# Kernel tuning notes

Measured on AMD Instinct MI355X. Metric: run time of the kernel, lower is better.

The kernel has to match this reference:

```python
import jax, jax.numpy as jnp
import numpy as np

N_NODES = 50000
N_EDGES = 800000
N_GRAPHS = 512
IN_CH, HID_CH, OUT_CH, N_CLASSES = 128, 64, 64, 10


def gcn_conv(x, src, dst, ew, W, b, n_nodes):
    """PyG GCNConv: add self-loops (weight 1), symmetric normalization, x @ W, scatter-add at dst, + bias."""
    xw = x @ W  # [N, out]
    loop = jnp.arange(n_nodes, dtype=src.dtype)
    src_f = jnp.concatenate([src, loop])
    dst_f = jnp.concatenate([dst, loop])
    ew_f = jnp.concatenate([ew, jnp.ones((n_nodes,), dtype=ew.dtype)])
    deg = jax.ops.segment_sum(ew_f, dst_f, num_segments=n_nodes)  # [N]
    dinv = jnp.where(deg > 0, jax.lax.rsqrt(deg), 0.0)
    norm = dinv[src_f] * ew_f * dinv[dst_f]  # [E+N]
    msg = norm[:, None] * xw[src_f]  # gather + scale
    out = jax.ops.segment_sum(msg, dst_f, num_segments=n_nodes)  # scatter-add
    return out + b


def setup_inputs() -> dict:
    key = jax.random.key(0)
    ks = jax.random.split(key, 12)
    x = jax.random.normal(ks[0], (N_NODES, IN_CH), dtype=jnp.float32)
    edge_index = jax.random.randint(ks[1], (2, N_EDGES), 0, N_NODES, dtype=jnp.int64)
    edge_attr = jax.random.uniform(ks[2], (N_EDGES,), dtype=jnp.float32)
    batch = jnp.sort(jax.random.randint(ks[3], (N_NODES,), 0, N_GRAPHS, dtype=jnp.int64))
    def glorot(k, shape):
        lim = np.sqrt(6.0 / (shape[0] + shape[1]))
        return jax.random.uniform(k, shape, jnp.float32, -lim, lim)
    W1 = glorot(ks[4], (IN_CH, HID_CH))
    b1 = jnp.zeros((HID_CH,), jnp.float32)
    W2 = glorot(ks[5], (HID_CH, OUT_CH))
    b2 = jnp.zeros((OUT_CH,), jnp.float32)
    LW1 = glorot(ks[6], (OUT_CH, 32))
    Lb1 = jnp.zeros((32,), jnp.float32)
    LW2 = glorot(ks[7], (32, N_CLASSES))
    Lb2 = jnp.zeros((N_CLASSES,), jnp.float32)
    return {"x": x, "edge_index": edge_index, "edge_attr": edge_attr, "batch": batch,
            "W1": W1, "b1": b1, "W2": W2, "b2": b2,
            "LW1": LW1, "Lb1": Lb1, "LW2": LW2, "Lb2": Lb2}


def reference(x, edge_index, edge_attr, batch, W1, b1, W2, b2, LW1, Lb1, LW2, Lb2):
    src, dst = edge_index[0], edge_index[1]
    h = gcn_conv(x, src, dst, edge_attr, W1, b1, N_NODES)
    h = jax.nn.relu(h)
    h = gcn_conv(h, src, dst, edge_attr, W2, b2, N_NODES)
    # global mean pool over graphs
    sums = jax.ops.segment_sum(h, batch, num_segments=N_GRAPHS)  # [G, OUT]
    cnt = jax.ops.segment_sum(jnp.ones((N_NODES,), h.dtype), batch, num_segments=N_GRAPHS)
    pooled = sums / jnp.maximum(cnt, 1.0)[:, None]
    # head (dropout treated as identity for deterministic reference)
    h1 = pooled @ LW1 + Lb1
    return h1 @ LW2 + Lb2
```

## Files before the change

### kernel.cpp

```cpp
#include <hip/hip_runtime.h>
#include <hip/hip_bf16.h>

static constexpr int NN = 50000;
static constexpr int NE = 800000;
static constexpr int NG = 512;
static constexpr int NB = 196;
static constexpr int GEMM_BLOCKS = (NN + 63) / 64;

__device__ __forceinline__ float bfu(ushort u) {
    return __uint_as_float((unsigned)u << 16);
}
__device__ __forceinline__ ushort fbf(float f) {
    return __hip_bfloat16_raw(__float2bfloat16(f)).x;
}


__global__ void zero_kernel(float* __restrict__ p, int n) {
    int i = blockIdx.x * blockDim.x + threadIdx.x;
    if (i < n) p[i] = 0.f;
}

template <int K, bool BF16IN>
__device__ __forceinline__ void gemm_body(const void* __restrict__ Xv,
                                          const float* __restrict__ W,
                                          ushort* __restrict__ out,
                                          int row0, float Xs[][68], float Ws[][64]) {
    int tx = threadIdx.x & 15, ty = threadIdx.x >> 4;
    float acc[4][4] = {};
    for (int kb = 0; kb < K; kb += 64) {
        __syncthreads();
        for (int i = threadIdx.x; i < 1024; i += 256) {
            int kk = i >> 4, c4 = i & 15;
            *(float4*)&Ws[kk][c4 * 4] = *(const float4*)&W[(kb + kk) * 64 + c4 * 4];
        }
        if constexpr (BF16IN) {
            const ushort* X = (const ushort*)Xv;
            for (int i = threadIdx.x; i < 512; i += 256) {
                int r = i >> 3, g = i & 7;
                int gr = row0 + r; if (gr >= NN) gr = NN - 1;
                uint4 v = *(const uint4*)(X + (long long)gr * K + kb + g * 8);
                float4 f0, f1;
                f0.x = __uint_as_float(v.x << 16); f0.y = __uint_as_float(v.x & 0xffff0000u);
                f0.z = __uint_as_float(v.y << 16); f0.w = __uint_as_float(v.y & 0xffff0000u);
                f1.x = __uint_as_float(v.z << 16); f1.y = __uint_as_float(v.z & 0xffff0000u);
                f1.z = __uint_as_float(v.w << 16); f1.w = __uint_as_float(v.w & 0xffff0000u);
                *(float4*)&Xs[r][g * 8] = f0;
                *(float4*)&Xs[r][g * 8 + 4] = f1;
            }
        } else {
            const float* X = (const float*)Xv;
            for (int i = threadIdx.x; i < 1024; i += 256) {
                int r = i >> 4, k4 = i & 15;
                int gr = row0 + r; if (gr >= NN) gr = NN - 1;
                float4 v = *(const float4*)(X + (long long)gr * K + kb + k4 * 4);
                *(float4*)&Xs[r][k4 * 4] = v;
            }
        }
        __syncthreads();
#pragma unroll 16
        for (int k = 0; k < 64; ++k) {
            float4 wv = *(const float4*)&Ws[k][tx * 4];
            float x0 = Xs[ty * 4 + 0][k];
            float x1 = Xs[ty * 4 + 1][k];
            float x2 = Xs[ty * 4 + 2][k];
            float x3 = Xs[ty * 4 + 3][k];
            acc[0][0] = fmaf(x0, wv.x, acc[0][0]); acc[0][1] = fmaf(x0, wv.y, acc[0][1]);
            acc[0][2] = fmaf(x0, wv.z, acc[0][2]); acc[0][3] = fmaf(x0, wv.w, acc[0][3]);
            acc[1][0] = fmaf(x1, wv.x, acc[1][0]); acc[1][1] = fmaf(x1, wv.y, acc[1][1]);
            acc[1][2] = fmaf(x1, wv.z, acc[1][2]); acc[1][3] = fmaf(x1, wv.w, acc[1][3]);
            acc[2][0] = fmaf(x2, wv.x, acc[2][0]); acc[2][1] = fmaf(x2, wv.y, acc[2][1]);
            acc[2][2] = fmaf(x2, wv.z, acc[2][2]); acc[2][3] = fmaf(x2, wv.w, acc[2][3]);
            acc[3][0] = fmaf(x3, wv.x, acc[3][0]); acc[3][1] = fmaf(x3, wv.y, acc[3][1]);
            acc[3][2] = fmaf(x3, wv.z, acc[3][2]); acc[3][3] = fmaf(x3, wv.w, acc[3][3]);
        }
    }
#pragma unroll
    for (int j = 0; j < 4; ++j) {
        int r = row0 + ty * 4 + j;
        if (r < NN) {
            ushort4 sv;
            sv.x = fbf(acc[j][0]); sv.y = fbf(acc[j][1]);
            sv.z = fbf(acc[j][2]); sv.w = fbf(acc[j][3]);
            *(ushort4*)(out + (long long)r * 64 + tx * 4) = sv;
        }
    }
}

__global__ __launch_bounds__(256) void hist_gemm_kernel(const int* __restrict__ dst,
                                                        const float* __restrict__ ew,
                                                        unsigned long long* __restrict__ h,
                                                        int* __restrict__ rank,
                                                        const float* __restrict__ X,
                                                        const float* __restrict__ W,
                                                        ushort* __restrict__ out) {
    __shared__ float Xs[64][68];
    __shared__ float Ws[64][64];
    for (int e = blockIdx.x * 256 + threadIdx.x; e < NE; e += GEMM_BLOCKS * 256) {
        int d = dst[e];
        unsigned int fx = __float2uint_rn(ew[e] * 1048576.0f);
        unsigned long long pack = (1ULL << 40) | (unsigned long long)fx;
        unsigned long long old = atomicAdd(&h[d], pack);
        rank[e] = (int)(old >> 40);
    }
    gemm_body<128, false>(X, W, out, blockIdx.x * 64, Xs, Ws);
}

template <int K, bool BF16IN>
__global__ __launch_bounds__(256) void gemm_kernel(const void* __restrict__ Xv,
                                                   const float* __restrict__ W,
                                                   ushort* __restrict__ out) {
    __shared__ float Xs[64][68];
    __shared__ float Ws[64][64];
    gemm_body<K, BF16IN>(Xv, W, out, blockIdx.x * 64, Xs, Ws);
}

__global__ __launch_bounds__(256) void dinv_scanA_kernel(const unsigned long long* __restrict__ h,
                                                         float* __restrict__ dinv,
                                                         int* __restrict__ partial) {
    int i = blockIdx.x * 256 + threadIdx.x;
    int cnt = 0;
    if (i < NN) {
        unsigned long long v = h[i];
        cnt = (int)(v >> 40);
        float deg = (float)(v & ((1ULL << 40) - 1)) * (1.0f / 1048576.0f) + 1.0f;
        dinv[i] = 1.0f / sqrtf(deg);
    }
    __shared__ int wsum[4];
    int lane = threadIdx.x & 63, wid = threadIdx.x >> 6;
    int v = cnt;
#pragma unroll
    for (int off = 32; off > 0; off >>= 1) v += __shfl_down(v, (unsigned)off, 64);
    if (lane == 0) wsum[wid] = v;
    __syncthreads();
    if (threadIdx.x == 0) partial[blockIdx.x] = wsum[0] + wsum[1] + wsum[2] + wsum[3];
}

__device__ __forceinline__ int block_scan_inclusive(int v, int* wtot) {
    int lane = threadIdx.x & 63, wid = threadIdx.x >> 6;
    int inc = v;
#pragma unroll
    for (int off = 1; off < 64; off <<= 1) {
        int n = __shfl_up(inc, (unsigned)off, 64);
        if (lane >= off) inc += n;
    }
    if (lane == 63) wtot[wid] = inc;
    __syncthreads();
    int add = 0;
    for (int w = 0; w < wid; ++w) add += wtot[w];
    return inc + add;
}

__global__ __launch_bounds__(256) void scanC_bounds_kernel(const unsigned long long* __restrict__ h,
                                                           const int* __restrict__ partial,
                                                           int* __restrict__ rowptr,
                                                           const int* __restrict__ batch,
                                                           int* __restrict__ gbeg,
                                                           int* __restrict__ gend) {
    __shared__ int wtot[4];
    __shared__ int poff_s;
    int t = threadIdx.x;
    if (t < 64) {
        int s = 0;
        for (int i = t; i < (int)blockIdx.x; i += 64) s += partial[i];
#pragma unroll
        for (int off = 32; off > 0; off >>= 1) s += __shfl_down(s, (unsigned)off, 64);
        if (t == 0) poff_s = s;
    }
    int i = blockIdx.x * 256 + t;
    int v = (i < NN) ? (int)(h[i] >> 40) : 0;
    int incl = block_scan_inclusive(v, wtot);
    if (i < NN) {
        rowptr[i + 1] = poff_s + incl;
        int g = batch[i];
        if (i == 0 || batch[i - 1] != g) gbeg[g] = i;
        if (i == NN - 1 || batch[i + 1] != g) gend[g] = i + 1;
    }
    if (i == 0) rowptr[0] = 0;
}

__global__ __launch_bounds__(256) void scatter_kernel(const int* __restrict__ src,
                                                      const int* __restrict__ dst,
                                                      const float* __restrict__ ew,
                                                      const float* __restrict__ dinv,
                                                      const int* __restrict__ rowptr,
                                                      const int* __restrict__ rank,
                                                      int2* __restrict__ epack) {
    int e = blockIdx.x * blockDim.x + threadIdx.x;
    if (e >= NE) return;
    int s = src[e], d = dst[e];
    int pos = rowptr[d] + rank[e];
    float coef = dinv[s] * ew[e];
    epack[pos] = make_int2(s, __float_as_int(coef));
}

template <bool RELU>
__global__ __launch_bounds__(256) void agg_kernel(const ushort* __restrict__ xw,
                                                  const int* __restrict__ rowptr,
                                                  const int2* __restrict__ epack,
                                                  const float* __restrict__ dinv,
                                                  const float* __restrict__ bias,
                                                  ushort* __restrict__ out) {
    int node = blockIdx.x * 4 + (threadIdx.x >> 6);
    if (node >= NN) return;
    int lane = threadIdx.x & 63;
    int q = lane >> 4;
    int l = lane & 15;
    int beg = rowptr[node], end = rowptr[node + 1];
    float a0 = 0.f, a1 = 0.f, a2 = 0.f, a3 = 0.f;
    float b0 = 0.f, b1 = 0.f, b2 = 0.f, b3 = 0.f;
    int j = beg + q;
    for (; j + 4 < end; j += 8) {
        int2 pA = epack[j];
        int2 pB = epack[j + 4];
        ushort4 uA = *(const ushort4*)(xw + pA.x * 64 + 4 * l);
        ushort4 uB = *(const ushort4*)(xw + pB.x * 64 + 4 * l);
        float wA = __int_as_float(pA.y);
        float wB = __int_as_float(pB.y);
        a0 = fmaf(wA, bfu(uA.x), a0); a1 = fmaf(wA, bfu(uA.y), a1);
        a2 = fmaf(wA, bfu(uA.z), a2); a3 = fmaf(wA, bfu(uA.w), a3);
        b0 = fmaf(wB, bfu(uB.x), b0); b1 = fmaf(wB, bfu(uB.y), b1);
        b2 = fmaf(wB, bfu(uB.z), b2); b3 = fmaf(wB, bfu(uB.w), b3);
    }
    if (j < end) {
        int2 pA = epack[j];
        ushort4 uA = *(const ushort4*)(xw + pA.x * 64 + 4 * l);
        float wA = __int_as_float(pA.y);
        a0 = fmaf(wA, bfu(uA.x), a0); a1 = fmaf(wA, bfu(uA.y), a1);
        a2 = fmaf(wA, bfu(uA.z), a2); a3 = fmaf(wA, bfu(uA.w), a3);
    }
    a0 += b0; a1 += b1; a2 += b2; a3 += b3;
    a0 += __shfl_xor(a0, 16); a0 += __shfl_xor(a0, 32);
    a1 += __shfl_xor(a1, 16); a1 += __shfl_xor(a1, 32);
    a2 += __shfl_xor(a2, 16); a2 += __shfl_xor(a2, 32);
    a3 += __shfl_xor(a3, 16); a3 += __shfl_xor(a3, 32);
    if (q == 0) {
        float di = dinv[node];
        float d2 = di * di;
        ushort4 us = *(const ushort4*)(xw + node * 64 + 4 * l);
        float4 bv = *(const float4*)(bias + 4 * l);
        float o0 = fmaf(di, a0, fmaf(d2, bfu(us.x), bv.x));
        float o1 = fmaf(di, a1, fmaf(d2, bfu(us.y), bv.y));
        float o2 = fmaf(di, a2, fmaf(d2, bfu(us.z), bv.z));
        float o3 = fmaf(di, a3, fmaf(d2, bfu(us.w), bv.w));
        if (RELU) {
            o0 = fmaxf(o0, 0.f); o1 = fmaxf(o1, 0.f);
            o2 = fmaxf(o2, 0.f); o3 = fmaxf(o3, 0.f);
        }
        ushort4 sv;
        sv.x = fbf(o0); sv.y = fbf(o1); sv.z = fbf(o2); sv.w = fbf(o3);
        *(ushort4*)(out + node * 64 + 4 * l) = sv;
    }
}

__global__ __launch_bounds__(256) void poolhead_kernel(const ushort* __restrict__ h,
                                                       const int* __restrict__ gbeg,
                                                       const int* __restrict__ gend,
                                                       const float* __restrict__ LW1,
                                                       const float* __restrict__ Lb1,
                                                       const float* __restrict__ LW2,
                                                       const float* __restrict__ Lb2,
                                                       float* __restrict__ out) {
    __shared__ float pp[4][64];
    __shared__ float p[64];
    __shared__ float t1[32];
    int g = blockIdx.x, t = threadIdx.x;
    int lane = t & 63, wid = t >> 6;
    int b = gbeg[g], e = gend[g];
    float acc = 0.f;
    for (int i = b + wid; i < e; i += 4) acc += bfu(h[i * 64 + lane]);
    pp[wid][lane] = acc;
    __syncthreads();
    if (t < 64) {
        float s = pp[0][t] + pp[1][t] + pp[2][t] + pp[3][t];
        p[t] = s / fmaxf((float)(e - b), 1.0f);
    }
    __syncthreads();
    if (t < 32) {
        float a = Lb1[t];
#pragma unroll
        for (int k = 0; k < 64; ++k) a = fmaf(p[k], LW1[k * 32 + t], a);
        t1[t] = a;
    }
    __syncthreads();
    if (t < 10) {
        float a = Lb2[t];
#pragma unroll
        for (int j = 0; j < 32; ++j) a = fmaf(t1[j], LW2[j * 10 + t], a);
        out[g * 10 + t] = a;
    }
}


extern "C" void kernel_launch(void* const* d_in, const int* in_sizes, int n_in,
                              void* d_out, int out_size, void* d_ws, size_t ws_size,
                              hipStream_t stream) {
    const float* x     = (const float*)d_in[0];
    const int*   ei    = (const int*)d_in[1];
    const float* ew    = (const float*)d_in[2];
    const int*   batch = (const int*)d_in[3];
    const float* W1    = (const float*)d_in[4];
    const float* b1    = (const float*)d_in[5];
    const float* W2    = (const float*)d_in[6];
    const float* b2    = (const float*)d_in[7];
    const float* LW1   = (const float*)d_in[8];
    const float* Lb1   = (const float*)d_in[9];
    const float* LW2   = (const float*)d_in[10];
    const float* Lb2   = (const float*)d_in[11];

    const int* src = ei;
    const int* dst = ei + NE;

    float* ws = (float*)d_ws;
    unsigned long long* h64 = (unsigned long long*)ws;
    int*   gbeg   = (int*)(ws + 100096);
    int*   gend   = (int*)(ws + 100608);
    float* dinv   = ws + 101120;
    int*   rowptr = (int*)(ws + 151168);
    int*   partial= (int*)(ws + 201216);
    int2*  epack  = (int2*)(ws + 201472);
    ushort* xwA   = (ushort*)(ws + 1801472);
    ushort* h12   = (ushort*)(ws + 3401472);
    int*   rank   = (int*)(ws + 5001472);

    zero_kernel<<<(101120 + 255) / 256, 256, 0, stream>>>(ws, 101120);

    hist_gemm_kernel<<<GEMM_BLOCKS, 256, 0, stream>>>(dst, ew, h64, rank, x, W1, xwA);
    dinv_scanA_kernel<<<NB, 256, 0, stream>>>(h64, dinv, partial);
    scanC_bounds_kernel<<<NB, 256, 0, stream>>>(h64, partial, rowptr, batch, gbeg, gend);
    scatter_kernel<<<(NE + 255) / 256, 256, 0, stream>>>(src, dst, ew, dinv, rowptr, rank, epack);

    agg_kernel<true><<<(NN + 3) / 4, 256, 0, stream>>>(xwA, rowptr, epack, dinv, b1, h12);

    gemm_kernel<64, true><<<GEMM_BLOCKS, 256, 0, stream>>>(h12, W2, xwA);
    agg_kernel<false><<<(NN + 3) / 4, 256, 0, stream>>>(xwA, rowptr, epack, dinv, b2, h12);

    poolhead_kernel<<<NG, 256, 0, stream>>>(h12, gbeg, gend, LW1, Lb1, LW2, Lb2, (float*)d_out);
}
```

Measured before the change: 247.6 us.

## Split histogram and GEMM into separate block roles and vectorize GEMM LDS reads

The fused histogram+GEMM kernel now gives the edge histogram atomics to a dedicated set of 128 blocks and the first-layer GEMM to the remaining blocks. Before, every GEMM block first ran its strided share of the atomics. The split lets the atomic-heavy and compute-heavy work run concurrently on different CUs instead of serializing inside each block. The GEMM inner loop also reads X from shared memory as float4 over four k values at a time, cutting LDS instruction count at the cost of more registers.

```diff
diff --git a/kernel.cpp b/kernel.cpp
--- a/kernel.cpp
+++ b/kernel.cpp
@@ -6,6 +6,7 @@
 static constexpr int NG = 512;
 static constexpr int NB = 196;
 static constexpr int GEMM_BLOCKS = (NN + 63) / 64;
+static constexpr int HB = 128;
 
 __device__ __forceinline__ float bfu(ushort u) {
     return __uint_as_float((unsigned)u << 16);
@@ -57,21 +58,30 @@
             }
         }
         __syncthreads();
-#pragma unroll 16
-        for (int k = 0; k < 64; ++k) {
-            float4 wv = *(const float4*)&Ws[k][tx * 4];
-            float x0 = Xs[ty * 4 + 0][k];
-            float x1 = Xs[ty * 4 + 1][k];
-            float x2 = Xs[ty * 4 + 2][k];
-            float x3 = Xs[ty * 4 + 3][k];
-            acc[0][0] = fmaf(x0, wv.x, acc[0][0]); acc[0][1] = fmaf(x0, wv.y, acc[0][1]);
-            acc[0][2] = fmaf(x0, wv.z, acc[0][2]); acc[0][3] = fmaf(x0, wv.w, acc[0][3]);
-            acc[1][0] = fmaf(x1, wv.x, acc[1][0]); acc[1][1] = fmaf(x1, wv.y, acc[1][1]);
-            acc[1][2] = fmaf(x1, wv.z, acc[1][2]); acc[1][3] = fmaf(x1, wv.w, acc[1][3]);
-            acc[2][0] = fmaf(x2, wv.x, acc[2][0]); acc[2][1] = fmaf(x2, wv.y, acc[2][1]);
-            acc[2][2] = fmaf(x2, wv.z, acc[2][2]); acc[2][3] = fmaf(x2, wv.w, acc[2][3]);
-            acc[3][0] = fmaf(x3, wv.x, acc[3][0]); acc[3][1] = fmaf(x3, wv.y, acc[3][1]);
-            acc[3][2] = fmaf(x3, wv.z, acc[3][2]); acc[3][3] = fmaf(x3, wv.w, acc[3][3]);
+#pragma unroll
+        for (int k4 = 0; k4 < 16; ++k4) {
+            float4 w0 = *(const float4*)&Ws[k4 * 4 + 0][tx * 4];
+            float4 w1 = *(const float4*)&Ws[k4 * 4 + 1][tx * 4];
+            float4 w2 = *(const float4*)&Ws[k4 * 4 + 2][tx * 4];
+            float4 w3 = *(const float4*)&Ws[k4 * 4 + 3][tx * 4];
+            float4 x0 = *(const float4*)&Xs[ty * 4 + 0][k4 * 4];
+            float4 x1 = *(const float4*)&Xs[ty * 4 + 1][k4 * 4];
+            float4 x2 = *(const float4*)&Xs[ty * 4 + 2][k4 * 4];
+            float4 x3 = *(const float4*)&Xs[ty * 4 + 3][k4 * 4];
+#define GCN_ROW(j, xv) \
+            acc[j][0]=fmaf(xv.x,w0.x,acc[j][0]); acc[j][1]=fmaf(xv.x,w0.y,acc[j][1]); \
+            acc[j][2]=fmaf(xv.x,w0.z,acc[j][2]); acc[j][3]=fmaf(xv.x,w0.w,acc[j][3]); \
+            acc[j][0]=fmaf(xv.y,w1.x,acc[j][0]); acc[j][1]=fmaf(xv.y,w1.y,acc[j][1]); \
+            acc[j][2]=fmaf(xv.y,w1.z,acc[j][2]); acc[j][3]=fmaf(xv.y,w1.w,acc[j][3]); \
+            acc[j][0]=fmaf(xv.z,w2.x,acc[j][0]); acc[j][1]=fmaf(xv.z,w2.y,acc[j][1]); \
+            acc[j][2]=fmaf(xv.z,w2.z,acc[j][2]); acc[j][3]=fmaf(xv.z,w2.w,acc[j][3]); \
+            acc[j][0]=fmaf(xv.w,w3.x,acc[j][0]); acc[j][1]=fmaf(xv.w,w3.y,acc[j][1]); \
+            acc[j][2]=fmaf(xv.w,w3.z,acc[j][2]); acc[j][3]=fmaf(xv.w,w3.w,acc[j][3]);
+            GCN_ROW(0, x0)
+            GCN_ROW(1, x1)
+            GCN_ROW(2, x2)
+            GCN_ROW(3, x3)
+#undef GCN_ROW
         }
     }
 #pragma unroll
@@ -95,14 +105,17 @@
                                                         ushort* __restrict__ out) {
     __shared__ float Xs[64][68];
     __shared__ float Ws[64][64];
-    for (int e = blockIdx.x * 256 + threadIdx.x; e < NE; e += GEMM_BLOCKS * 256) {
-        int d = dst[e];
-        unsigned int fx = __float2uint_rn(ew[e] * 1048576.0f);
-        unsigned long long pack = (1ULL << 40) | (unsigned long long)fx;
-        unsigned long long old = atomicAdd(&h[d], pack);
-        rank[e] = (int)(old >> 40);
-    }
-    gemm_body<128, false>(X, W, out, blockIdx.x * 64, Xs, Ws);
+    if (blockIdx.x < HB) {
+        for (int e = blockIdx.x * 256 + threadIdx.x; e < NE; e += HB * 256) {
+            int d = dst[e];
+            unsigned int fx = __float2uint_rn(ew[e] * 1048576.0f);
+            unsigned long long pack = (1ULL << 40) | (unsigned long long)fx;
+            unsigned long long old = atomicAdd(&h[d], pack);
+            rank[e] = (int)(old >> 40);
+        }
+        return;
+    }
+    gemm_body<128, false>(X, W, out, (blockIdx.x - HB) * 64, Xs, Ws);
 }
 
 template <int K, bool BF16IN>
@@ -324,7 +337,7 @@
 
     zero_kernel<<<(101120 + 255) / 256, 256, 0, stream>>>(ws, 101120);
 
-    hist_gemm_kernel<<<GEMM_BLOCKS, 256, 0, stream>>>(dst, ew, h64, rank, x, W1, xwA);
+    hist_gemm_kernel<<<HB + GEMM_BLOCKS, 256, 0, stream>>>(dst, ew, h64, rank, x, W1, xwA);
     dinv_scanA_kernel<<<NB, 256, 0, stream>>>(h64, dinv, partial);
     scanC_bounds_kernel<<<NB, 256, 0, stream>>>(h64, partial, rowptr, batch, gbeg, gend);
     scatter_kernel<<<(NE + 255) / 256, 256, 0, stream>>>(src, dst, ew, dinv, rowptr, rank, epack);
```

Measured after the change: 243.7 us. Within noise of the previous version (-1.6%).
